# Kernel tuning notes

Hardware: AMD Instinct MI355X
Metric: run time of the kernel (lower is better)

## Reference

```python
import jax, jax.numpy as jnp
import numpy as np

N = 210          # sequence length (== module max_length cap)
DM = 2048        # input feature dim (major and minor)
DK = 1024        # key/query dim
DV = 1024        # value dim
K_CLIP = 32      # relative-position clipping distance


def _make_table(n, k):
    # table[i, j] = clip(j - i, -k, k) + k  (Shaw-style relative position index)
    rel = np.arange(n)[None, :] - np.arange(n)[:, None]
    return jnp.asarray(np.clip(rel, -k, k) + k, dtype=jnp.int32)


def setup_inputs() -> dict:
    key = jax.random.key(0)
    ks = jax.random.split(key, 7)
    X_major = jax.random.normal(ks[0], (N, DM), dtype=jnp.float32)
    X_minor = jax.random.normal(ks[1], (N, DM), dtype=jnp.float32)
    # Linear weights stored as [in, out] for x @ W
    s = 0.02
    Wq = jax.random.normal(ks[2], (DM, DK), dtype=jnp.float32) * s
    Wk = jax.random.normal(ks[3], (DM, DK), dtype=jnp.float32) * s
    Wv = jax.random.normal(ks[4], (DM, DV), dtype=jnp.float32) * s
    Wo = jax.random.normal(ks[5], (DV, DV), dtype=jnp.float32) * s
    wk = jax.random.normal(ks[6], (2 * K_CLIP + 1, DK), dtype=jnp.float32) * s
    table = _make_table(N, K_CLIP)
    return {"X_major": X_major, "X_minor": X_minor, "Wq": Wq, "Wk": Wk,
            "Wv": Wv, "Wo": Wo, "wk": wk, "table": table}


def reference(X_major, X_minor, Wq, Wk, Wv, Wo, wk, table):
    n = X_major.shape[0]
    scale = 1.0 / jnp.sqrt(jnp.asarray(Wq.shape[1], X_major.dtype))
    Q = X_major @ Wq                     # [n, dk]
    K = X_minor @ Wk                     # [n, dk]
    V = X_minor @ Wv                     # [n, dv]
    Qs = Q * scale
    S = Qs @ K.T                         # [n, n] content scores
    Rk = wk[table[:n, :n]]               # [n, n, dk] gathered rel-pos reps
    Sr = jnp.einsum('id,ijd->ij', Qs, Rk)  # [n, n] relative scores
    A = jax.nn.softmax(S + Sr, axis=-1)  # [n, n]
    Y = (A @ V) @ Wo                     # [n, dv]
    return (Y, A)
```

## Files before the change

### kernel.cpp

```cpp
#include <hip/hip_runtime.h>

typedef short bf16x8 __attribute__((ext_vector_type(8)));
typedef float f32x4 __attribute__((ext_vector_type(4)));

#define MFMA16(a, b, c) __builtin_amdgcn_mfma_f32_16x16x32_bf16(a, b, c, 0, 0, 0)

__device__ inline short f2bf(float f) {
  unsigned u = __builtin_bit_cast(unsigned, f);
  u += 0x7FFFu + ((u >> 16) & 1u);
  return (short)(u >> 16);
}
__device__ inline unsigned pack2(float lo, float hi) {
  unsigned a = __builtin_bit_cast(unsigned, lo) + 0x8000u;
  unsigned b = __builtin_bit_cast(unsigned, hi) + 0x8000u;
  return __builtin_amdgcn_perm(b, a, 0x07060302u);
}

__device__ inline void async_cp16(const void* g, void* l) {
  __builtin_amdgcn_global_load_lds(
      (const __attribute__((address_space(1))) unsigned int*)g,
      (__attribute__((address_space(3))) unsigned int*)l, 16, 0, 0);
}

#define SWZ(r, c) ((((r) << 4) + ((c) ^ ((r) & 7))) << 3)


__global__ __launch_bounds__(256) void k_prep(const float* __restrict__ xmaj,
                                              const float* __restrict__ xmin,
                                              const float* __restrict__ wkin,
                                              const float* __restrict__ Wq,
                                              const float* __restrict__ Wk,
                                              const float* __restrict__ Wv,
                                              const float* __restrict__ Wo,
                                              short* __restrict__ xmaj_bf,
                                              short* __restrict__ xmin_bf,
                                              short* __restrict__ kwb,
                                              short* __restrict__ wqt,
                                              short* __restrict__ wkt,
                                              short* __restrict__ wvt,
                                              short* __restrict__ wot) {
  __shared__ short tile[64][72];
  int b = blockIdx.x, t = threadIdx.x;
  if (b < 512) {
    int idx = b * 256 + t;
    if (idx < 107520) {
      float4 v = ((const float4*)xmaj)[idx];
      ((uint2*)xmaj_bf)[idx] = make_uint2(pack2(v.x, v.y), pack2(v.z, v.w));
      float4 u = ((const float4*)xmin)[idx];
      ((uint2*)xmin_bf)[idx] = make_uint2(pack2(u.x, u.y), pack2(u.z, u.w));
    }
    if (idx < 16640) {
      float4 v = ((const float4*)wkin)[idx];
      ((uint2*)(kwb + 210 * 1024))[idx] = make_uint2(pack2(v.x, v.y), pack2(v.z, v.w));
    }
    if (idx < 1664) ((uint4*)(kwb + 275 * 1024))[idx] = make_uint4(0, 0, 0, 0);
    return;
  }
  const float* W;
  short* Wt;
  int kt, nt, dstK;
  if (b < 2048) {
    int wi = (b - 512) >> 9, tl = (b - 512) & 511;
    W = wi == 0 ? Wq : (wi == 1 ? Wk : Wv);
    Wt = wi == 0 ? wqt : (wi == 1 ? wkt : wvt);
    kt = tl >> 4; nt = tl & 15; dstK = 2048;
  } else {
    int tl = b - 2048;
    W = Wo; Wt = wot; kt = tl >> 4; nt = tl & 15; dstK = 1024;
  }
  int k0 = kt * 64, n0 = nt * 64;
  int kp = t >> 4, nl4 = (t & 15) * 4;
  for (int h = 0; h < 2; ++h) {
    int kpp = kp + h * 16;
    const float* g = W + (size_t)(k0 + 2 * kpp) * 1024 + n0 + nl4;
    float4 u = *(const float4*)g;
    float4 v = *(const float4*)(g + 1024);
    *(unsigned*)&tile[nl4 + 0][2 * kpp] = pack2(u.x, v.x);
    *(unsigned*)&tile[nl4 + 1][2 * kpp] = pack2(u.y, v.y);
    *(unsigned*)&tile[nl4 + 2][2 * kpp] = pack2(u.z, v.z);
    *(unsigned*)&tile[nl4 + 3][2 * kpp] = pack2(u.w, v.w);
  }
  __syncthreads();
  int nl = t >> 2, cq = t & 3;
  for (int h = 0; h < 2; ++h) {
    int c = cq + h * 4;
    *(uint4*)(Wt + (size_t)(n0 + nl) * dstK + k0 + c * 8) = *(const uint4*)&tile[nl][c * 8];
  }
}

__global__ __launch_bounds__(256, 1) void k_qkv(const short* __restrict__ xmaj,
                                                const short* __restrict__ xmin,
                                                const short* __restrict__ wqt,
                                                const short* __restrict__ wkt,
                                                const short* __restrict__ wvt,
                                                short* __restrict__ qs,
                                                short* __restrict__ kwb,
                                                short* __restrict__ vt) {
  __shared__ short As[64 * 128];
  __shared__ short Bs[64 * 128];
  int b = blockIdx.x, t = threadIdx.x;
  int x = b & 7, s = b >> 3;
  int ntile = x * 6 + (s >> 2), mtile = s & 3;
  int nn0 = ntile * 64;
  int mat = nn0 >> 10, ncol0 = nn0 & 1023, m0 = mtile * 64;
  const short* A = (mat == 0) ? xmaj : xmin;
  const short* Bt = (mat == 0) ? wqt : (mat == 1 ? wkt : wvt);
  int lane = t & 63, w = t >> 6;
  int wm = w >> 1, wn = w & 1;
  int l15 = lane & 15, l4 = lane >> 4;
  f32x4 acc[2][2] = {};

  for (int k0 = 0; k0 < 2048; k0 += 128) {
    __syncthreads();
#pragma unroll
    for (int j = 0; j < 4; ++j) {
      int sj = t + j * 256;
      int r = sj >> 4, cg = (sj & 15) ^ (r & 7);
      async_cp16(A + (size_t)(m0 + r) * 2048 + k0 + cg * 8, &As[(w * 64 + j * 256) * 8]);
    }
#pragma unroll
    for (int j = 0; j < 4; ++j) {
      int sj = t + j * 256;
      int r = sj >> 4, cg = (sj & 15) ^ (r & 7);
      async_cp16(Bt + (size_t)(ncol0 + r) * 2048 + k0 + cg * 8, &Bs[(w * 64 + j * 256) * 8]);
    }
    __syncthreads();
#pragma unroll
    for (int kk = 0; kk < 4; ++kk) {
      int c = kk * 4 + l4;
      int ra0 = wm * 32 + l15, ra1 = ra0 + 16;
      int rb0 = wn * 32 + l15, rb1 = rb0 + 16;
      bf16x8 a0 = *(const bf16x8*)&As[SWZ(ra0, c)];
      bf16x8 a1 = *(const bf16x8*)&As[SWZ(ra1, c)];
      bf16x8 b0 = *(const bf16x8*)&Bs[SWZ(rb0, c)];
      bf16x8 b1 = *(const bf16x8*)&Bs[SWZ(rb1, c)];
      acc[0][0] = MFMA16(a0, b0, acc[0][0]);
      acc[0][1] = MFMA16(a0, b1, acc[0][1]);
      acc[1][0] = MFMA16(a1, b0, acc[1][0]);
      acc[1][1] = MFMA16(a1, b1, acc[1][1]);
    }
  }

  if (mat < 2) {
    float scale = (mat == 0) ? 0.03125f : 1.0f;
    short* dst = (mat == 0) ? qs : kwb;
#pragma unroll
    for (int mi = 0; mi < 2; ++mi)
#pragma unroll
      for (int ni = 0; ni < 2; ++ni) {
        int r0 = m0 + wm * 32 + mi * 16 + l4 * 4;
        int c = ncol0 + wn * 32 + ni * 16 + l15;
        for (int j = 0; j < 4; ++j) {
          int r = r0 + j;
          if (r < 210) dst[r * 1024 + c] = f2bf(acc[mi][ni][j] * scale);
        }
      }
  } else {
    __syncthreads();
#pragma unroll
    for (int mi = 0; mi < 2; ++mi)
#pragma unroll
      for (int ni = 0; ni < 2; ++ni) {
        int nl = wn * 32 + ni * 16 + l15;
        int ml0 = wm * 32 + mi * 16 + l4 * 4;
        for (int j = 0; j < 4; ++j) As[nl * 72 + ml0 + j] = f2bf(acc[mi][ni][j]);
      }
    __syncthreads();
    for (int h = 0; h < 2; ++h) {
      int idx = t + h * 256;
      int nl = idx >> 3, c8 = idx & 7;
      int mg0 = m0 + c8 * 8;
      short* dstp = vt + (ncol0 + nl) * 256 + mg0;
      if (mg0 + 8 <= 210) {
        *(uint4*)dstp = *(const uint4*)&As[nl * 72 + c8 * 8];
      } else {
        for (int e = 0; e < 8; ++e)
          if (mg0 + e < 210) dstp[e] = As[nl * 72 + c8 * 8 + e];
      }
    }
  }
}

__global__ __launch_bounds__(256, 1) void k_sprime(const short* __restrict__ qs,
                                                   const short* __restrict__ kwb,
                                                   float* __restrict__ Sp) {
  __shared__ short As[32 * 128];
  __shared__ short Bs[64 * 128];
  int n0 = blockIdx.x * 64, m0 = blockIdx.y * 32;
  int t = threadIdx.x, lane = t & 63, w = t >> 6;
  int l15 = lane & 15, l4 = lane >> 4;
  f32x4 acc[2] = {};

  for (int k0 = 0; k0 < 1024; k0 += 128) {
    __syncthreads();
#pragma unroll
    for (int j = 0; j < 2; ++j) {
      int sj = t + j * 256;
      int r = sj >> 4, cg = (sj & 15) ^ (r & 7);
      async_cp16(qs + (size_t)(m0 + r) * 1024 + k0 + cg * 8, &As[(w * 64 + j * 256) * 8]);
    }
#pragma unroll
    for (int j = 0; j < 4; ++j) {
      int sj = t + j * 256;
      int r = sj >> 4, cg = (sj & 15) ^ (r & 7);
      async_cp16(kwb + (size_t)(n0 + r) * 1024 + k0 + cg * 8, &Bs[(w * 64 + j * 256) * 8]);
    }
    __syncthreads();
#pragma unroll
    for (int kk = 0; kk < 4; ++kk) {
      int c = kk * 4 + l4;
      int rb = w * 16 + l15;
      bf16x8 a0 = *(const bf16x8*)&As[SWZ(l15, c)];
      bf16x8 a1 = *(const bf16x8*)&As[SWZ(16 + l15, c)];
      bf16x8 bb = *(const bf16x8*)&Bs[SWZ(rb, c)];
      acc[0] = MFMA16(a0, bb, acc[0]);
      acc[1] = MFMA16(a1, bb, acc[1]);
    }
  }
#pragma unroll
  for (int mi = 0; mi < 2; ++mi) {
    int r0 = m0 + mi * 16 + l4 * 4;
    int col = n0 + w * 16 + l15;
    for (int j = 0; j < 4; ++j) Sp[(r0 + j) * 320 + col] = acc[mi][j];
  }
}

__global__ __launch_bounds__(256) void k_softmax(const float* __restrict__ Sp,
                                                 const int* __restrict__ table,
                                                 short* __restrict__ Abf,
                                                 float* __restrict__ outA) {
  int i = blockIdx.x, t = threadIdx.x;
  if (i >= 210) {
    Abf[i * 256 + t] = 0;
    return;
  }
  __shared__ float srow[288];
  __shared__ float red[4];
  for (int j = t; j < 288; j += 256) srow[j] = Sp[i * 320 + j];
  __syncthreads();
  float logit = -1e30f;
  if (t < 210) {
    int tb = table[i * 210 + t];
    logit = srow[t] + srow[210 + tb];
  }
  float m = logit;
  for (int o = 32; o; o >>= 1) m = fmaxf(m, __shfl_xor(m, o));
  if ((t & 63) == 0) red[t >> 6] = m;
  __syncthreads();
  m = fmaxf(fmaxf(red[0], red[1]), fmaxf(red[2], red[3]));
  float e = (t < 210) ? __expf(logit - m) : 0.0f;
  float s = e;
  for (int o = 32; o; o >>= 1) s += __shfl_xor(s, o);
  __syncthreads();
  if ((t & 63) == 0) red[t >> 6] = s;
  __syncthreads();
  s = red[0] + red[1] + red[2] + red[3];
  float a = e / s;
  Abf[i * 256 + t] = (t < 210) ? f2bf(a) : (short)0;
  if (t < 210) outA[i * 210 + t] = a;
}

__global__ __launch_bounds__(256, 1) void k_av(const short* __restrict__ Abf,
                                               const short* __restrict__ vt,
                                               short* __restrict__ av) {
  __shared__ short As[64 * 128];
  __shared__ short Bs[64 * 128];
  int n0 = blockIdx.x * 64, m0 = blockIdx.y * 64;
  int t = threadIdx.x, lane = t & 63, w = t >> 6;
  int wm = w >> 1, wn = w & 1;
  int l15 = lane & 15, l4 = lane >> 4;
  f32x4 acc[2][2] = {};

  for (int k0 = 0; k0 < 256; k0 += 128) {
    __syncthreads();
#pragma unroll
    for (int j = 0; j < 4; ++j) {
      int sj = t + j * 256;
      int r = sj >> 4, cg = (sj & 15) ^ (r & 7);
      async_cp16(Abf + (size_t)(m0 + r) * 256 + k0 + cg * 8, &As[(w * 64 + j * 256) * 8]);
      async_cp16(vt + (size_t)(n0 + r) * 256 + k0 + cg * 8, &Bs[(w * 64 + j * 256) * 8]);
    }
    __syncthreads();
#pragma unroll
    for (int kk = 0; kk < 4; ++kk) {
      int c = kk * 4 + l4;
      int ra0 = wm * 32 + l15, ra1 = ra0 + 16;
      int rb0 = wn * 32 + l15, rb1 = rb0 + 16;
      bf16x8 a0 = *(const bf16x8*)&As[SWZ(ra0, c)];
      bf16x8 a1 = *(const bf16x8*)&As[SWZ(ra1, c)];
      bf16x8 b0 = *(const bf16x8*)&Bs[SWZ(rb0, c)];
      bf16x8 b1 = *(const bf16x8*)&Bs[SWZ(rb1, c)];
      acc[0][0] = MFMA16(a0, b0, acc[0][0]);
      acc[0][1] = MFMA16(a0, b1, acc[0][1]);
      acc[1][0] = MFMA16(a1, b0, acc[1][0]);
      acc[1][1] = MFMA16(a1, b1, acc[1][1]);
    }
  }
#pragma unroll
  for (int mi = 0; mi < 2; ++mi)
#pragma unroll
    for (int ni = 0; ni < 2; ++ni) {
      int r0 = m0 + wm * 32 + mi * 16 + l4 * 4;
      int c = n0 + wn * 32 + ni * 16 + l15;
      for (int j = 0; j < 4; ++j) {
        int r = r0 + j;
        if (r < 210) av[r * 1024 + c] = f2bf(acc[mi][ni][j]);
      }
    }
}

__global__ __launch_bounds__(256, 1) void k_y(const short* __restrict__ av,
                                              const short* __restrict__ wot,
                                              float* __restrict__ outY) {
  __shared__ short As[64 * 128];
  __shared__ short Bs[64 * 128];
  int n0 = blockIdx.x * 64, m0 = blockIdx.y * 64;
  int t = threadIdx.x, lane = t & 63, w = t >> 6;
  int wm = w >> 1, wn = w & 1;
  int l15 = lane & 15, l4 = lane >> 4;
  f32x4 acc[2][2] = {};

  for (int k0 = 0; k0 < 1024; k0 += 128) {
    __syncthreads();
#pragma unroll
    for (int j = 0; j < 4; ++j) {
      int sj = t + j * 256;
      int r = sj >> 4, cg = (sj & 15) ^ (r & 7);
      async_cp16(av + (size_t)(m0 + r) * 1024 + k0 + cg * 8, &As[(w * 64 + j * 256) * 8]);
      async_cp16(wot + (size_t)(n0 + r) * 1024 + k0 + cg * 8, &Bs[(w * 64 + j * 256) * 8]);
    }
    __syncthreads();
#pragma unroll
    for (int kk = 0; kk < 4; ++kk) {
      int c = kk * 4 + l4;
      int ra0 = wm * 32 + l15, ra1 = ra0 + 16;
      int rb0 = wn * 32 + l15, rb1 = rb0 + 16;
      bf16x8 a0 = *(const bf16x8*)&As[SWZ(ra0, c)];
      bf16x8 a1 = *(const bf16x8*)&As[SWZ(ra1, c)];
      bf16x8 b0 = *(const bf16x8*)&Bs[SWZ(rb0, c)];
      bf16x8 b1 = *(const bf16x8*)&Bs[SWZ(rb1, c)];
      acc[0][0] = MFMA16(a0, b0, acc[0][0]);
      acc[0][1] = MFMA16(a0, b1, acc[0][1]);
      acc[1][0] = MFMA16(a1, b0, acc[1][0]);
      acc[1][1] = MFMA16(a1, b1, acc[1][1]);
    }
  }
#pragma unroll
  for (int mi = 0; mi < 2; ++mi)
#pragma unroll
    for (int ni = 0; ni < 2; ++ni) {
      int r0 = m0 + wm * 32 + mi * 16 + l4 * 4;
      int c = n0 + wn * 32 + ni * 16 + l15;
      for (int j = 0; j < 4; ++j) {
        int r = r0 + j;
        if (r < 210) outY[r * 1024 + c] = acc[mi][ni][j];
      }
    }
}

extern "C" void kernel_launch(void* const* d_in, const int* in_sizes, int n_in,
                              void* d_out, int out_size, void* d_ws, size_t ws_size,
                              hipStream_t stream) {
  const float* Xmaj = (const float*)d_in[0];
  const float* Xmin = (const float*)d_in[1];
  const float* Wq = (const float*)d_in[2];
  const float* Wk = (const float*)d_in[3];
  const float* Wv = (const float*)d_in[4];
  const float* Wo = (const float*)d_in[5];
  const float* wk = (const float*)d_in[6];
  const int* table = (const int*)d_in[7];

  char* ws = (char*)d_ws;
  short* xmaj_bf = (short*)(ws + 0);
  short* xmin_bf = (short*)(ws + 1048576);
  short* qs = (short*)(ws + 2097152);
  short* kwb = (short*)(ws + 2621440);
  short* vt = (short*)(ws + 3276800);
  short* Abf = (short*)(ws + 3801088);
  short* av = (short*)(ws + 3932160);
  float* Sp = (float*)(ws + 4456448);
  short* wqt = (short*)(ws + 4743168);
  short* wkt = (short*)(ws + 8937472);
  short* wvt = (short*)(ws + 13131776);
  short* wot = (short*)(ws + 17326080);

  float* outY = (float*)d_out;
  float* outA = (float*)d_out + 215040;

  k_prep<<<2304, 256, 0, stream>>>(Xmaj, Xmin, wk, Wq, Wk, Wv, Wo,
                                   xmaj_bf, xmin_bf, kwb, wqt, wkt, wvt, wot);
  k_qkv<<<192, 256, 0, stream>>>(xmaj_bf, xmin_bf, wqt, wkt, wvt, qs, kwb, vt);
  k_sprime<<<dim3(5, 7), 256, 0, stream>>>(qs, kwb, Sp);
  k_softmax<<<256, 256, 0, stream>>>(Sp, table, Abf, outA);
  k_av<<<dim3(16, 4), 256, 0, stream>>>(Abf, vt, av);
  k_y<<<dim3(16, 4), 256, 0, stream>>>(av, wot, outY);
}
```

Baseline: 127.0 us.

## Fuse softmax into AV GEMM and double K-tile depth to 256

Removes the separate softmax kernel. Each AV block now computes the softmax rows for its 64-row tile directly from Sp and the table, writes them into LDS as bf16, and writes the fp32 A output only from the blocks with n0==0. All GEMM kernels (qkv, sprime, y) also move from 128-wide to 256-wide K tiles, using a new 32-chunk swizzle, which halves the number of loop iterations and barriers. In exchange, each of the 16 column blocks recomputes softmax for its rows, and LDS use per block grows considerably (about 118KB in the fused kernel).

```diff
diff --git a/kernel.cpp b/kernel.cpp
--- a/kernel.cpp
+++ b/kernel.cpp
@@ -15,14 +15,14 @@
   unsigned b = __builtin_bit_cast(unsigned, hi) + 0x8000u;
   return __builtin_amdgcn_perm(b, a, 0x07060302u);
 }
-
 __device__ inline void async_cp16(const void* g, void* l) {
   __builtin_amdgcn_global_load_lds(
       (const __attribute__((address_space(1))) unsigned int*)g,
       (__attribute__((address_space(3))) unsigned int*)l, 16, 0, 0);
 }
-
-#define SWZ(r, c) ((((r) << 4) + ((c) ^ ((r) & 7))) << 3)
+__device__ inline int swz5(int r, int c) {
+  return ((r << 5) + ((c & ~7) | ((c ^ r) & 7))) << 3;
+}
 
 
 __global__ __launch_bounds__(256) void k_prep(const float* __restrict__ xmaj,
@@ -96,8 +96,8 @@
                                                 short* __restrict__ qs,
                                                 short* __restrict__ kwb,
                                                 short* __restrict__ vt) {
-  __shared__ short As[64 * 128];
-  __shared__ short Bs[64 * 128];
+  __shared__ short As[64 * 256];
+  __shared__ short Bs[64 * 256];
   int b = blockIdx.x, t = threadIdx.x;
   int x = b & 7, s = b >> 3;
   int ntile = x * 6 + (s >> 2), mtile = s & 3;
@@ -110,30 +110,32 @@
   int l15 = lane & 15, l4 = lane >> 4;
   f32x4 acc[2][2] = {};
 
-  for (int k0 = 0; k0 < 2048; k0 += 128) {
-    __syncthreads();
-#pragma unroll
-    for (int j = 0; j < 4; ++j) {
+  for (int k0 = 0; k0 < 2048; k0 += 256) {
+    __syncthreads();
+#pragma unroll
+    for (int j = 0; j < 8; ++j) {
       int sj = t + j * 256;
-      int r = sj >> 4, cg = (sj & 15) ^ (r & 7);
-      async_cp16(A + (size_t)(m0 + r) * 2048 + k0 + cg * 8, &As[(w * 64 + j * 256) * 8]);
-    }
-#pragma unroll
-    for (int j = 0; j < 4; ++j) {
+      int r = sj >> 5, c = sj & 31;
+      int cg = (c & ~7) | ((c ^ r) & 7);
+      async_cp16(A + (size_t)(m0 + r) * 2048 + k0 + cg * 8, &As[(j * 256 + w * 64) * 8]);
+    }
+#pragma unroll
+    for (int j = 0; j < 8; ++j) {
       int sj = t + j * 256;
-      int r = sj >> 4, cg = (sj & 15) ^ (r & 7);
-      async_cp16(Bt + (size_t)(ncol0 + r) * 2048 + k0 + cg * 8, &Bs[(w * 64 + j * 256) * 8]);
-    }
-    __syncthreads();
-#pragma unroll
-    for (int kk = 0; kk < 4; ++kk) {
+      int r = sj >> 5, c = sj & 31;
+      int cg = (c & ~7) | ((c ^ r) & 7);
+      async_cp16(Bt + (size_t)(ncol0 + r) * 2048 + k0 + cg * 8, &Bs[(j * 256 + w * 64) * 8]);
+    }
+    __syncthreads();
+#pragma unroll
+    for (int kk = 0; kk < 8; ++kk) {
       int c = kk * 4 + l4;
       int ra0 = wm * 32 + l15, ra1 = ra0 + 16;
       int rb0 = wn * 32 + l15, rb1 = rb0 + 16;
-      bf16x8 a0 = *(const bf16x8*)&As[SWZ(ra0, c)];
-      bf16x8 a1 = *(const bf16x8*)&As[SWZ(ra1, c)];
-      bf16x8 b0 = *(const bf16x8*)&Bs[SWZ(rb0, c)];
-      bf16x8 b1 = *(const bf16x8*)&Bs[SWZ(rb1, c)];
+      bf16x8 a0 = *(const bf16x8*)&As[swz5(ra0, c)];
+      bf16x8 a1 = *(const bf16x8*)&As[swz5(ra1, c)];
+      bf16x8 b0 = *(const bf16x8*)&Bs[swz5(rb0, c)];
+      bf16x8 b1 = *(const bf16x8*)&Bs[swz5(rb1, c)];
       acc[0][0] = MFMA16(a0, b0, acc[0][0]);
       acc[0][1] = MFMA16(a0, b1, acc[0][1]);
       acc[1][0] = MFMA16(a1, b0, acc[1][0]);
@@ -184,35 +186,36 @@
 __global__ __launch_bounds__(256, 1) void k_sprime(const short* __restrict__ qs,
                                                    const short* __restrict__ kwb,
                                                    float* __restrict__ Sp) {
-  __shared__ short As[32 * 128];
-  __shared__ short Bs[64 * 128];
+  __shared__ short As2[32 * 256];
+  __shared__ short Bs2[64 * 256];
   int n0 = blockIdx.x * 64, m0 = blockIdx.y * 32;
   int t = threadIdx.x, lane = t & 63, w = t >> 6;
   int l15 = lane & 15, l4 = lane >> 4;
   f32x4 acc[2] = {};
 
-  for (int k0 = 0; k0 < 1024; k0 += 128) {
-    __syncthreads();
-#pragma unroll
-    for (int j = 0; j < 2; ++j) {
-      int sj = t + j * 256;
-      int r = sj >> 4, cg = (sj & 15) ^ (r & 7);
-      async_cp16(qs + (size_t)(m0 + r) * 1024 + k0 + cg * 8, &As[(w * 64 + j * 256) * 8]);
-    }
+  for (int k0 = 0; k0 < 1024; k0 += 256) {
+    __syncthreads();
 #pragma unroll
     for (int j = 0; j < 4; ++j) {
       int sj = t + j * 256;
-      int r = sj >> 4, cg = (sj & 15) ^ (r & 7);
-      async_cp16(kwb + (size_t)(n0 + r) * 1024 + k0 + cg * 8, &Bs[(w * 64 + j * 256) * 8]);
-    }
-    __syncthreads();
-#pragma unroll
-    for (int kk = 0; kk < 4; ++kk) {
+      int r = sj >> 5, c = sj & 31;
+      int cg = (c & ~7) | ((c ^ r) & 7);
+      async_cp16(qs + (size_t)(m0 + r) * 1024 + k0 + cg * 8, &As2[(j * 256 + w * 64) * 8]);
+    }
+#pragma unroll
+    for (int j = 0; j < 8; ++j) {
+      int sj = t + j * 256;
+      int r = sj >> 5, c = sj & 31;
+      int cg = (c & ~7) | ((c ^ r) & 7);
+      async_cp16(kwb + (size_t)(n0 + r) * 1024 + k0 + cg * 8, &Bs2[(j * 256 + w * 64) * 8]);
+    }
+    __syncthreads();
+#pragma unroll
+    for (int kk = 0; kk < 8; ++kk) {
       int c = kk * 4 + l4;
-      int rb = w * 16 + l15;
-      bf16x8 a0 = *(const bf16x8*)&As[SWZ(l15, c)];
-      bf16x8 a1 = *(const bf16x8*)&As[SWZ(16 + l15, c)];
-      bf16x8 bb = *(const bf16x8*)&Bs[SWZ(rb, c)];
+      bf16x8 a0 = *(const bf16x8*)&As2[swz5(l15, c)];
+      bf16x8 a1 = *(const bf16x8*)&As2[swz5(16 + l15, c)];
+      bf16x8 bb = *(const bf16x8*)&Bs2[swz5(w * 16 + l15, c)];
       acc[0] = MFMA16(a0, bb, acc[0]);
       acc[1] = MFMA16(a1, bb, acc[1]);
     }
@@ -225,120 +228,123 @@
   }
 }
 
-__global__ __launch_bounds__(256) void k_softmax(const float* __restrict__ Sp,
-                                                 const int* __restrict__ table,
-                                                 short* __restrict__ Abf,
-                                                 float* __restrict__ outA) {
-  int i = blockIdx.x, t = threadIdx.x;
-  if (i >= 210) {
-    Abf[i * 256 + t] = 0;
-    return;
-  }
-  __shared__ float srow[288];
-  __shared__ float red[4];
-  for (int j = t; j < 288; j += 256) srow[j] = Sp[i * 320 + j];
+__global__ __launch_bounds__(256, 1) void k_av_smax(const float* __restrict__ Sp,
+                                                    const int* __restrict__ table,
+                                                    const short* __restrict__ vt,
+                                                    short* __restrict__ av,
+                                                    float* __restrict__ outA) {
+  __shared__ short As[64 * 256];
+  __shared__ short Bs[64 * 256];
+  __shared__ float Ls[64 * 212];
+  int n0 = blockIdx.x * 64, m0 = blockIdx.y * 64;
+  int t = threadIdx.x, lane = t & 63, w = t >> 6;
+  int wm = w >> 1, wn = w & 1;
+  int l15 = lane & 15, l4 = lane >> 4;
+
+#pragma unroll
+  for (int j = 0; j < 8; ++j) {
+    int sj = t + j * 256;
+    int r = sj >> 5, c = sj & 31;
+    int cg = (c & ~7) | ((c ^ r) & 7);
+    async_cp16(vt + (size_t)(n0 + r) * 256 + cg * 8, &Bs[(j * 256 + w * 64) * 8]);
+  }
+
+  int r = t >> 2, q = t & 3;
+  int row = m0 + r;
+  float* Lr = Ls + r * 212;
+  if (row < 210) {
+    const float* sp = Sp + (size_t)row * 320;
+    const int* tr = table + (size_t)row * 210;
+    float mx = -1e30f;
+    for (int j = q; j < 210; j += 4) {
+      int tb = tr[j];
+      float lg = sp[j] + sp[210 + tb];
+      Lr[j] = lg;
+      mx = fmaxf(mx, lg);
+    }
+    for (int o = 2; o; o >>= 1) mx = fmaxf(mx, __shfl_xor(mx, o, 4));
+    float sum = 0.0f;
+    for (int j = q; j < 210; j += 4) {
+      float e = __expf(Lr[j] - mx);
+      Lr[j] = e;
+      sum += e;
+    }
+    for (int o = 2; o; o >>= 1) sum += __shfl_xor(sum, o, 4);
+    float inv = 1.0f / sum;
+    bool wA = (n0 == 0);
+    for (int j = q; j < 256; j += 4) {
+      if (j < 210) {
+        float a = Lr[j] * inv;
+        As[swz5(r, j >> 3) + (j & 7)] = f2bf(a);
+        if (wA) outA[(size_t)row * 210 + j] = a;
+      } else {
+        As[swz5(r, j >> 3) + (j & 7)] = 0;
+      }
+    }
+  } else {
+    for (int j = q; j < 256; j += 4) As[swz5(r, j >> 3) + (j & 7)] = 0;
+  }
   __syncthreads();
-  float logit = -1e30f;
-  if (t < 210) {
-    int tb = table[i * 210 + t];
-    logit = srow[t] + srow[210 + tb];
-  }
-  float m = logit;
-  for (int o = 32; o; o >>= 1) m = fmaxf(m, __shfl_xor(m, o));
-  if ((t & 63) == 0) red[t >> 6] = m;
-  __syncthreads();
-  m = fmaxf(fmaxf(red[0], red[1]), fmaxf(red[2], red[3]));
-  float e = (t < 210) ? __expf(logit - m) : 0.0f;
-  float s = e;
-  for (int o = 32; o; o >>= 1) s += __shfl_xor(s, o);
-  __syncthreads();
-  if ((t & 63) == 0) red[t >> 6] = s;
-  __syncthreads();
-  s = red[0] + red[1] + red[2] + red[3];
-  float a = e / s;
-  Abf[i * 256 + t] = (t < 210) ? f2bf(a) : (short)0;
-  if (t < 210) outA[i * 210 + t] = a;
-}
-
-__global__ __launch_bounds__(256, 1) void k_av(const short* __restrict__ Abf,
-                                               const short* __restrict__ vt,
-                                               short* __restrict__ av) {
-  __shared__ short As[64 * 128];
-  __shared__ short Bs[64 * 128];
+
+  f32x4 acc[2][2] = {};
+#pragma unroll
+  for (int kk = 0; kk < 8; ++kk) {
+    int c = kk * 4 + l4;
+    int ra0 = wm * 32 + l15, ra1 = ra0 + 16;
+    int rb0 = wn * 32 + l15, rb1 = rb0 + 16;
+    bf16x8 a0 = *(const bf16x8*)&As[swz5(ra0, c)];
+    bf16x8 a1 = *(const bf16x8*)&As[swz5(ra1, c)];
+    bf16x8 b0 = *(const bf16x8*)&Bs[swz5(rb0, c)];
+    bf16x8 b1 = *(const bf16x8*)&Bs[swz5(rb1, c)];
+    acc[0][0] = MFMA16(a0, b0, acc[0][0]);
+    acc[0][1] = MFMA16(a0, b1, acc[0][1]);
+    acc[1][0] = MFMA16(a1, b0, acc[1][0]);
+    acc[1][1] = MFMA16(a1, b1, acc[1][1]);
+  }
+#pragma unroll
+  for (int mi = 0; mi < 2; ++mi)
+#pragma unroll
+    for (int ni = 0; ni < 2; ++ni) {
+      int r0 = m0 + wm * 32 + mi * 16 + l4 * 4;
+      int c = n0 + wn * 32 + ni * 16 + l15;
+      for (int j = 0; j < 4; ++j) {
+        int rr = r0 + j;
+        if (rr < 210) av[rr * 1024 + c] = f2bf(acc[mi][ni][j]);
+      }
+    }
+}
+
+__global__ __launch_bounds__(256, 1) void k_y(const short* __restrict__ av,
+                                              const short* __restrict__ wot,
+                                              float* __restrict__ outY) {
+  __shared__ short As[64 * 256];
+  __shared__ short Bs[64 * 256];
   int n0 = blockIdx.x * 64, m0 = blockIdx.y * 64;
   int t = threadIdx.x, lane = t & 63, w = t >> 6;
   int wm = w >> 1, wn = w & 1;
   int l15 = lane & 15, l4 = lane >> 4;
   f32x4 acc[2][2] = {};
 
-  for (int k0 = 0; k0 < 256; k0 += 128) {
-    __syncthreads();
-#pragma unroll
-    for (int j = 0; j < 4; ++j) {
+  for (int k0 = 0; k0 < 1024; k0 += 256) {
+    __syncthreads();
+#pragma unroll
+    for (int j = 0; j < 8; ++j) {
       int sj = t + j * 256;
-      int r = sj >> 4, cg = (sj & 15) ^ (r & 7);
-      async_cp16(Abf + (size_t)(m0 + r) * 256 + k0 + cg * 8, &As[(w * 64 + j * 256) * 8]);
-      async_cp16(vt + (size_t)(n0 + r) * 256 + k0 + cg * 8, &Bs[(w * 64 + j * 256) * 8]);
-    }
-    __syncthreads();
-#pragma unroll
-    for (int kk = 0; kk < 4; ++kk) {
+      int r = sj >> 5, c = sj & 31;
+      int cg = (c & ~7) | ((c ^ r) & 7);
+      async_cp16(av + (size_t)(m0 + r) * 1024 + k0 + cg * 8, &As[(j * 256 + w * 64) * 8]);
+      async_cp16(wot + (size_t)(n0 + r) * 1024 + k0 + cg * 8, &Bs[(j * 256 + w * 64) * 8]);
+    }
+    __syncthreads();
+#pragma unroll
+    for (int kk = 0; kk < 8; ++kk) {
       int c = kk * 4 + l4;
       int ra0 = wm * 32 + l15, ra1 = ra0 + 16;
       int rb0 = wn * 32 + l15, rb1 = rb0 + 16;
-      bf16x8 a0 = *(const bf16x8*)&As[SWZ(ra0, c)];
-      bf16x8 a1 = *(const bf16x8*)&As[SWZ(ra1, c)];
-      bf16x8 b0 = *(const bf16x8*)&Bs[SWZ(rb0, c)];
-      bf16x8 b1 = *(const bf16x8*)&Bs[SWZ(rb1, c)];
-      acc[0][0] = MFMA16(a0, b0, acc[0][0]);
-      acc[0][1] = MFMA16(a0, b1, acc[0][1]);
-      acc[1][0] = MFMA16(a1, b0, acc[1][0]);
-      acc[1][1] = MFMA16(a1, b1, acc[1][1]);
-    }
-  }
-#pragma unroll
-  for (int mi = 0; mi < 2; ++mi)
-#pragma unroll
-    for (int ni = 0; ni < 2; ++ni) {
-      int r0 = m0 + wm * 32 + mi * 16 + l4 * 4;
-      int c = n0 + wn * 32 + ni * 16 + l15;
-      for (int j = 0; j < 4; ++j) {
-        int r = r0 + j;
-        if (r < 210) av[r * 1024 + c] = f2bf(acc[mi][ni][j]);
-      }
-    }
-}
-
-__global__ __launch_bounds__(256, 1) void k_y(const short* __restrict__ av,
-                                              const short* __restrict__ wot,
-                                              float* __restrict__ outY) {
-  __shared__ short As[64 * 128];
-  __shared__ short Bs[64 * 128];
-  int n0 = blockIdx.x * 64, m0 = blockIdx.y * 64;
-  int t = threadIdx.x, lane = t & 63, w = t >> 6;
-  int wm = w >> 1, wn = w & 1;
-  int l15 = lane & 15, l4 = lane >> 4;
-  f32x4 acc[2][2] = {};
-
-  for (int k0 = 0; k0 < 1024; k0 += 128) {
-    __syncthreads();
-#pragma unroll
-    for (int j = 0; j < 4; ++j) {
-      int sj = t + j * 256;
-      int r = sj >> 4, cg = (sj & 15) ^ (r & 7);
-      async_cp16(av + (size_t)(m0 + r) * 1024 + k0 + cg * 8, &As[(w * 64 + j * 256) * 8]);
-      async_cp16(wot + (size_t)(n0 + r) * 1024 + k0 + cg * 8, &Bs[(w * 64 + j * 256) * 8]);
-    }
-    __syncthreads();
-#pragma unroll
-    for (int kk = 0; kk < 4; ++kk) {
-      int c = kk * 4 + l4;
-      int ra0 = wm * 32 + l15, ra1 = ra0 + 16;
-      int rb0 = wn * 32 + l15, rb1 = rb0 + 16;
-      bf16x8 a0 = *(const bf16x8*)&As[SWZ(ra0, c)];
-      bf16x8 a1 = *(const bf16x8*)&As[SWZ(ra1, c)];
-      bf16x8 b0 = *(const bf16x8*)&Bs[SWZ(rb0, c)];
-      bf16x8 b1 = *(const bf16x8*)&Bs[SWZ(rb1, c)];
+      bf16x8 a0 = *(const bf16x8*)&As[swz5(ra0, c)];
+      bf16x8 a1 = *(const bf16x8*)&As[swz5(ra1, c)];
+      bf16x8 b0 = *(const bf16x8*)&Bs[swz5(rb0, c)];
+      bf16x8 b1 = *(const bf16x8*)&Bs[swz5(rb1, c)];
       acc[0][0] = MFMA16(a0, b0, acc[0][0]);
       acc[0][1] = MFMA16(a0, b1, acc[0][1]);
       acc[1][0] = MFMA16(a1, b0, acc[1][0]);
@@ -376,7 +382,6 @@
   short* qs = (short*)(ws + 2097152);
   short* kwb = (short*)(ws + 2621440);
   short* vt = (short*)(ws + 3276800);
-  short* Abf = (short*)(ws + 3801088);
   short* av = (short*)(ws + 3932160);
   float* Sp = (float*)(ws + 4456448);
   short* wqt = (short*)(ws + 4743168);
@@ -391,7 +396,6 @@
                                    xmaj_bf, xmin_bf, kwb, wqt, wkt, wvt, wot);
   k_qkv<<<192, 256, 0, stream>>>(xmaj_bf, xmin_bf, wqt, wkt, wvt, qs, kwb, vt);
   k_sprime<<<dim3(5, 7), 256, 0, stream>>>(qs, kwb, Sp);
-  k_softmax<<<256, 256, 0, stream>>>(Sp, table, Abf, outA);
-  k_av<<<dim3(16, 4), 256, 0, stream>>>(Abf, vt, av);
+  k_av_smax<<<dim3(16, 4), 256, 0, stream>>>(Sp, table, vt, av, outA);
   k_y<<<dim3(16, 4), 256, 0, stream>>>(av, wot, outY);
 }
```

Result: slower. 150.9 us (+18.8%).

## Fuse fp32-to-bf16 conversion into QKV GEMM and double-buffer GEMM loads

Applied to the files above, without the earlier changes.

Removes the separate prep kernel. The QKV GEMM now loads fp32 X and W tiles straight into LDS with async copies, converts them to bf16 in-kernel, and transposes W through LDS. Extra blocks of the same launch handle the wk conversion and the Wo transpose. The sprime and y kernels gain double-buffered LDS prefetch, and k_av loads its whole K=256 extent in one shot. This avoids a full fp32-to-bf16 round trip through global memory for the large weights, at the cost of more LDS use and conversion work repeated inside each GEMM block.

```diff
diff --git a/kernel.cpp b/kernel.cpp
--- a/kernel.cpp
+++ b/kernel.cpp
@@ -15,129 +15,146 @@
   unsigned b = __builtin_bit_cast(unsigned, hi) + 0x8000u;
   return __builtin_amdgcn_perm(b, a, 0x07060302u);
 }
-
 __device__ inline void async_cp16(const void* g, void* l) {
   __builtin_amdgcn_global_load_lds(
       (const __attribute__((address_space(1))) unsigned int*)g,
       (__attribute__((address_space(3))) unsigned int*)l, 16, 0, 0);
 }
-
 #define SWZ(r, c) ((((r) << 4) + ((c) ^ ((r) & 7))) << 3)
-
-
-__global__ __launch_bounds__(256) void k_prep(const float* __restrict__ xmaj,
-                                              const float* __restrict__ xmin,
-                                              const float* __restrict__ wkin,
-                                              const float* __restrict__ Wq,
-                                              const float* __restrict__ Wk,
-                                              const float* __restrict__ Wv,
-                                              const float* __restrict__ Wo,
-                                              short* __restrict__ xmaj_bf,
-                                              short* __restrict__ xmin_bf,
-                                              short* __restrict__ kwb,
-                                              short* __restrict__ wqt,
-                                              short* __restrict__ wkt,
-                                              short* __restrict__ wvt,
-                                              short* __restrict__ wot) {
-  __shared__ short tile[64][72];
-  int b = blockIdx.x, t = threadIdx.x;
-  if (b < 512) {
-    int idx = b * 256 + t;
-    if (idx < 107520) {
-      float4 v = ((const float4*)xmaj)[idx];
-      ((uint2*)xmaj_bf)[idx] = make_uint2(pack2(v.x, v.y), pack2(v.z, v.w));
-      float4 u = ((const float4*)xmin)[idx];
-      ((uint2*)xmin_bf)[idx] = make_uint2(pack2(u.x, u.y), pack2(u.z, u.w));
-    }
-    if (idx < 16640) {
-      float4 v = ((const float4*)wkin)[idx];
-      ((uint2*)(kwb + 210 * 1024))[idx] = make_uint2(pack2(v.x, v.y), pack2(v.z, v.w));
-    }
-    if (idx < 1664) ((uint4*)(kwb + 275 * 1024))[idx] = make_uint4(0, 0, 0, 0);
-    return;
-  }
-  const float* W;
-  short* Wt;
-  int kt, nt, dstK;
-  if (b < 2048) {
-    int wi = (b - 512) >> 9, tl = (b - 512) & 511;
-    W = wi == 0 ? Wq : (wi == 1 ? Wk : Wv);
-    Wt = wi == 0 ? wqt : (wi == 1 ? wkt : wvt);
-    kt = tl >> 4; nt = tl & 15; dstK = 2048;
-  } else {
-    int tl = b - 2048;
-    W = Wo; Wt = wot; kt = tl >> 4; nt = tl & 15; dstK = 1024;
-  }
-  int k0 = kt * 64, n0 = nt * 64;
-  int kp = t >> 4, nl4 = (t & 15) * 4;
-  for (int h = 0; h < 2; ++h) {
-    int kpp = kp + h * 16;
-    const float* g = W + (size_t)(k0 + 2 * kpp) * 1024 + n0 + nl4;
-    float4 u = *(const float4*)g;
-    float4 v = *(const float4*)(g + 1024);
-    *(unsigned*)&tile[nl4 + 0][2 * kpp] = pack2(u.x, v.x);
-    *(unsigned*)&tile[nl4 + 1][2 * kpp] = pack2(u.y, v.y);
-    *(unsigned*)&tile[nl4 + 2][2 * kpp] = pack2(u.z, v.z);
-    *(unsigned*)&tile[nl4 + 3][2 * kpp] = pack2(u.w, v.w);
-  }
-  __syncthreads();
-  int nl = t >> 2, cq = t & 3;
-  for (int h = 0; h < 2; ++h) {
-    int c = cq + h * 4;
-    *(uint4*)(Wt + (size_t)(n0 + nl) * dstK + k0 + c * 8) = *(const uint4*)&tile[nl][c * 8];
-  }
-}
-
-__global__ __launch_bounds__(256, 1) void k_qkv(const short* __restrict__ xmaj,
-                                                const short* __restrict__ xmin,
-                                                const short* __restrict__ wqt,
-                                                const short* __restrict__ wkt,
-                                                const short* __restrict__ wvt,
+__device__ inline int swz5(int r, int c) {
+  return ((r << 5) + ((c & ~7) | ((c ^ r) & 7))) << 3;
+}
+__device__ inline int xsw(int r, int c) { return (c & ~7) | ((c ^ r) & 7); }
+
+
+__global__ __launch_bounds__(256, 1) void k_qkv(const float* __restrict__ xmaj,
+                                                const float* __restrict__ xmin,
+                                                const float* __restrict__ Wq,
+                                                const float* __restrict__ Wk,
+                                                const float* __restrict__ Wv,
+                                                const float* __restrict__ Wo,
+                                                const float* __restrict__ wkin,
                                                 short* __restrict__ qs,
                                                 short* __restrict__ kwb,
-                                                short* __restrict__ vt) {
-  __shared__ short As[64 * 128];
+                                                short* __restrict__ vt,
+                                                short* __restrict__ wot) {
+  __shared__ float Xs[2][64 * 128];
+  __shared__ float Ws[2][128 * 64];
   __shared__ short Bs[64 * 128];
   int b = blockIdx.x, t = threadIdx.x;
+
+  if (b >= 192) {
+    if (b < 194) {
+      int idx = (b - 192) * 256 + t;
+      const float4* src = (const float4*)wkin;
+      uint2* dst = (uint2*)(kwb + 210 * 1024);
+      for (int i = idx; i < 16640; i += 512) {
+        float4 v = src[i];
+        dst[i] = make_uint2(pack2(v.x, v.y), pack2(v.z, v.w));
+      }
+      for (int i = idx; i < 1664; i += 512)
+        ((uint4*)(kwb + 275 * 1024))[i] = make_uint4(0, 0, 0, 0);
+    } else {
+      short(*tile)[72] = (short(*)[72])Bs;
+      int tl = b - 194;
+      int k0 = (tl >> 4) * 64, n0 = (tl & 15) * 64;
+      int kp = t >> 4, nl4 = (t & 15) * 4;
+#pragma unroll
+      for (int h = 0; h < 2; ++h) {
+        int kpp = kp + h * 16;
+        const float* g = Wo + (size_t)(k0 + 2 * kpp) * 1024 + n0 + nl4;
+        float4 u = *(const float4*)g;
+        float4 v = *(const float4*)(g + 1024);
+        *(unsigned*)&tile[nl4 + 0][2 * kpp] = pack2(u.x, v.x);
+        *(unsigned*)&tile[nl4 + 1][2 * kpp] = pack2(u.y, v.y);
+        *(unsigned*)&tile[nl4 + 2][2 * kpp] = pack2(u.z, v.z);
+        *(unsigned*)&tile[nl4 + 3][2 * kpp] = pack2(u.w, v.w);
+      }
+      __syncthreads();
+      int nl = t >> 2, cq = t & 3;
+#pragma unroll
+      for (int h = 0; h < 2; ++h) {
+        int c = cq + h * 4;
+        *(uint4*)(wot + (size_t)(n0 + nl) * 1024 + k0 + c * 8) = *(const uint4*)&tile[nl][c * 8];
+      }
+    }
+    return;
+  }
+
   int x = b & 7, s = b >> 3;
   int ntile = x * 6 + (s >> 2), mtile = s & 3;
   int nn0 = ntile * 64;
   int mat = nn0 >> 10, ncol0 = nn0 & 1023, m0 = mtile * 64;
-  const short* A = (mat == 0) ? xmaj : xmin;
-  const short* Bt = (mat == 0) ? wqt : (mat == 1 ? wkt : wvt);
+  const float* Xa = (mat == 0) ? xmaj : xmin;
+  const float* Wp = (mat == 0) ? Wq : (mat == 1 ? Wk : Wv);
   int lane = t & 63, w = t >> 6;
   int wm = w >> 1, wn = w & 1;
   int l15 = lane & 15, l4 = lane >> 4;
   f32x4 acc[2][2] = {};
 
-  for (int k0 = 0; k0 < 2048; k0 += 128) {
+  auto issue = [&](int p) {
+    int k0 = p * 128;
+    float* X = &Xs[p & 1][0];
+    float* W2 = &Ws[p & 1][0];
+#pragma unroll
+    for (int j = 0; j < 8; ++j) {
+      int sj = t + j * 256;
+      int r = sj >> 5, c = sj & 31;
+      int row = m0 + r;
+      row = row > 209 ? 209 : row;
+      async_cp16(Xa + (size_t)row * 2048 + k0 + xsw(r, c) * 4, &X[(j * 256 + w * 64) * 4]);
+    }
+#pragma unroll
+    for (int j = 0; j < 8; ++j) {
+      int sj = t + j * 256;
+      int r = sj >> 4, c = sj & 15;
+      async_cp16(Wp + (size_t)(k0 + r) * 1024 + ncol0 + xsw(r, c) * 4, &W2[(j * 256 + w * 64) * 4]);
+    }
+  };
+
+  issue(0);
+#pragma unroll 1
+  for (int p = 0; p < 16; ++p) {
     __syncthreads();
-#pragma unroll
-    for (int j = 0; j < 4; ++j) {
-      int sj = t + j * 256;
-      int r = sj >> 4, cg = (sj & 15) ^ (r & 7);
-      async_cp16(A + (size_t)(m0 + r) * 2048 + k0 + cg * 8, &As[(w * 64 + j * 256) * 8]);
-    }
-#pragma unroll
-    for (int j = 0; j < 4; ++j) {
-      int sj = t + j * 256;
-      int r = sj >> 4, cg = (sj & 15) ^ (r & 7);
-      async_cp16(Bt + (size_t)(ncol0 + r) * 2048 + k0 + cg * 8, &Bs[(w * 64 + j * 256) * 8]);
-    }
-    __syncthreads();
-#pragma unroll
-    for (int kk = 0; kk < 4; ++kk) {
-      int c = kk * 4 + l4;
-      int ra0 = wm * 32 + l15, ra1 = ra0 + 16;
-      int rb0 = wn * 32 + l15, rb1 = rb0 + 16;
-      bf16x8 a0 = *(const bf16x8*)&As[SWZ(ra0, c)];
-      bf16x8 a1 = *(const bf16x8*)&As[SWZ(ra1, c)];
-      bf16x8 b0 = *(const bf16x8*)&Bs[SWZ(rb0, c)];
-      bf16x8 b1 = *(const bf16x8*)&Bs[SWZ(rb1, c)];
-      acc[0][0] = MFMA16(a0, b0, acc[0][0]);
-      acc[0][1] = MFMA16(a0, b1, acc[0][1]);
-      acc[1][0] = MFMA16(a1, b0, acc[1][0]);
-      acc[1][1] = MFMA16(a1, b1, acc[1][1]);
+    if (p < 15) issue(p + 1);
+    {
+      const float* W2 = &Ws[p & 1][0];
+#pragma unroll
+      for (int h = 0; h < 4; ++h) {
+        int kp = (t >> 4) + 16 * h, nq = t & 15;
+        int r0 = 2 * kp, r1 = r0 + 1;
+        float4 u = *(const float4*)&W2[r0 * 64 + xsw(r0, nq) * 4];
+        float4 v = *(const float4*)&W2[r1 * 64 + xsw(r1, nq) * 4];
+        int kc = kp >> 2, e = r0 & 7;
+        *(unsigned*)&Bs[SWZ(nq * 4 + 0, kc) + e] = pack2(u.x, v.x);
+        *(unsigned*)&Bs[SWZ(nq * 4 + 1, kc) + e] = pack2(u.y, v.y);
+        *(unsigned*)&Bs[SWZ(nq * 4 + 2, kc) + e] = pack2(u.z, v.z);
+        *(unsigned*)&Bs[SWZ(nq * 4 + 3, kc) + e] = pack2(u.w, v.w);
+      }
+    }
+    asm volatile("s_waitcnt lgkmcnt(0)\ns_barrier" ::: "memory");
+    {
+      const float* X = &Xs[p & 1][0];
+#pragma unroll
+      for (int kk = 0; kk < 4; ++kk) {
+        int c = kk * 4 + l4;
+        int ra0 = wm * 32 + l15, ra1 = ra0 + 16;
+        int rb0 = wn * 32 + l15, rb1 = rb0 + 16;
+        float4 u0 = *(const float4*)&X[ra0 * 128 + xsw(ra0, 2 * c) * 4];
+        float4 v0 = *(const float4*)&X[ra0 * 128 + xsw(ra0, 2 * c + 1) * 4];
+        float4 u1 = *(const float4*)&X[ra1 * 128 + xsw(ra1, 2 * c) * 4];
+        float4 v1 = *(const float4*)&X[ra1 * 128 + xsw(ra1, 2 * c + 1) * 4];
+        uint4 pa0 = make_uint4(pack2(u0.x, u0.y), pack2(u0.z, u0.w), pack2(v0.x, v0.y), pack2(v0.z, v0.w));
+        uint4 pa1 = make_uint4(pack2(u1.x, u1.y), pack2(u1.z, u1.w), pack2(v1.x, v1.y), pack2(v1.z, v1.w));
+        bf16x8 a0 = __builtin_bit_cast(bf16x8, pa0);
+        bf16x8 a1 = __builtin_bit_cast(bf16x8, pa1);
+        bf16x8 b0 = *(const bf16x8*)&Bs[SWZ(rb0, c)];
+        bf16x8 b1 = *(const bf16x8*)&Bs[SWZ(rb1, c)];
+        acc[0][0] = MFMA16(a0, b0, acc[0][0]);
+        acc[0][1] = MFMA16(a0, b1, acc[0][1]);
+        acc[1][0] = MFMA16(a1, b0, acc[1][0]);
+        acc[1][1] = MFMA16(a1, b1, acc[1][1]);
+      }
     }
   }
 
@@ -157,13 +174,14 @@
       }
   } else {
     __syncthreads();
+    short* scr = Bs;
 #pragma unroll
     for (int mi = 0; mi < 2; ++mi)
 #pragma unroll
       for (int ni = 0; ni < 2; ++ni) {
         int nl = wn * 32 + ni * 16 + l15;
         int ml0 = wm * 32 + mi * 16 + l4 * 4;
-        for (int j = 0; j < 4; ++j) As[nl * 72 + ml0 + j] = f2bf(acc[mi][ni][j]);
+        for (int j = 0; j < 4; ++j) scr[nl * 72 + ml0 + j] = f2bf(acc[mi][ni][j]);
       }
     __syncthreads();
     for (int h = 0; h < 2; ++h) {
@@ -172,10 +190,10 @@
       int mg0 = m0 + c8 * 8;
       short* dstp = vt + (ncol0 + nl) * 256 + mg0;
       if (mg0 + 8 <= 210) {
-        *(uint4*)dstp = *(const uint4*)&As[nl * 72 + c8 * 8];
+        *(uint4*)dstp = *(const uint4*)&scr[nl * 72 + c8 * 8];
       } else {
         for (int e = 0; e < 8; ++e)
-          if (mg0 + e < 210) dstp[e] = As[nl * 72 + c8 * 8 + e];
+          if (mg0 + e < 210) dstp[e] = scr[nl * 72 + c8 * 8 + e];
       }
     }
   }
@@ -184,35 +202,41 @@
 __global__ __launch_bounds__(256, 1) void k_sprime(const short* __restrict__ qs,
                                                    const short* __restrict__ kwb,
                                                    float* __restrict__ Sp) {
-  __shared__ short As[32 * 128];
-  __shared__ short Bs[64 * 128];
+  __shared__ short As[2][32 * 128];
+  __shared__ short Bs[2][64 * 128];
   int n0 = blockIdx.x * 64, m0 = blockIdx.y * 32;
   int t = threadIdx.x, lane = t & 63, w = t >> 6;
   int l15 = lane & 15, l4 = lane >> 4;
   f32x4 acc[2] = {};
 
-  for (int k0 = 0; k0 < 1024; k0 += 128) {
-    __syncthreads();
+  auto issue = [&](int p) {
+    int k0 = p * 128, d = p & 1;
 #pragma unroll
     for (int j = 0; j < 2; ++j) {
       int sj = t + j * 256;
       int r = sj >> 4, cg = (sj & 15) ^ (r & 7);
-      async_cp16(qs + (size_t)(m0 + r) * 1024 + k0 + cg * 8, &As[(w * 64 + j * 256) * 8]);
+      async_cp16(qs + (size_t)(m0 + r) * 1024 + k0 + cg * 8, &As[d][(j * 256 + w * 64) * 8]);
     }
 #pragma unroll
     for (int j = 0; j < 4; ++j) {
       int sj = t + j * 256;
       int r = sj >> 4, cg = (sj & 15) ^ (r & 7);
-      async_cp16(kwb + (size_t)(n0 + r) * 1024 + k0 + cg * 8, &Bs[(w * 64 + j * 256) * 8]);
-    }
+      async_cp16(kwb + (size_t)(n0 + r) * 1024 + k0 + cg * 8, &Bs[d][(j * 256 + w * 64) * 8]);
+    }
+  };
+
+  issue(0);
+#pragma unroll 1
+  for (int p = 0; p < 8; ++p) {
     __syncthreads();
+    if (p < 7) issue(p + 1);
+    int d = p & 1;
 #pragma unroll
     for (int kk = 0; kk < 4; ++kk) {
       int c = kk * 4 + l4;
-      int rb = w * 16 + l15;
-      bf16x8 a0 = *(const bf16x8*)&As[SWZ(l15, c)];
-      bf16x8 a1 = *(const bf16x8*)&As[SWZ(16 + l15, c)];
-      bf16x8 bb = *(const bf16x8*)&Bs[SWZ(rb, c)];
+      bf16x8 a0 = *(const bf16x8*)&As[d][SWZ(l15, c)];
+      bf16x8 a1 = *(const bf16x8*)&As[d][SWZ(16 + l15, c)];
+      bf16x8 bb = *(const bf16x8*)&Bs[d][SWZ(w * 16 + l15, c)];
       acc[0] = MFMA16(a0, bb, acc[0]);
       acc[1] = MFMA16(a1, bb, acc[1]);
     }
@@ -263,38 +287,37 @@
 __global__ __launch_bounds__(256, 1) void k_av(const short* __restrict__ Abf,
                                                const short* __restrict__ vt,
                                                short* __restrict__ av) {
-  __shared__ short As[64 * 128];
-  __shared__ short Bs[64 * 128];
+  __shared__ short As[64 * 256];
+  __shared__ short Bs[64 * 256];
   int n0 = blockIdx.x * 64, m0 = blockIdx.y * 64;
   int t = threadIdx.x, lane = t & 63, w = t >> 6;
   int wm = w >> 1, wn = w & 1;
   int l15 = lane & 15, l4 = lane >> 4;
+
+#pragma unroll
+  for (int j = 0; j < 8; ++j) {
+    int sj = t + j * 256;
+    int r = sj >> 5, c = sj & 31;
+    int cg = (c & ~7) | ((c ^ r) & 7);
+    async_cp16(Abf + (size_t)(m0 + r) * 256 + cg * 8, &As[(j * 256 + w * 64) * 8]);
+    async_cp16(vt + (size_t)(n0 + r) * 256 + cg * 8, &Bs[(j * 256 + w * 64) * 8]);
+  }
+  __syncthreads();
+
   f32x4 acc[2][2] = {};
-
-  for (int k0 = 0; k0 < 256; k0 += 128) {
-    __syncthreads();
-#pragma unroll
-    for (int j = 0; j < 4; ++j) {
-      int sj = t + j * 256;
-      int r = sj >> 4, cg = (sj & 15) ^ (r & 7);
-      async_cp16(Abf + (size_t)(m0 + r) * 256 + k0 + cg * 8, &As[(w * 64 + j * 256) * 8]);
-      async_cp16(vt + (size_t)(n0 + r) * 256 + k0 + cg * 8, &Bs[(w * 64 + j * 256) * 8]);
-    }
-    __syncthreads();
-#pragma unroll
-    for (int kk = 0; kk < 4; ++kk) {
-      int c = kk * 4 + l4;
-      int ra0 = wm * 32 + l15, ra1 = ra0 + 16;
-      int rb0 = wn * 32 + l15, rb1 = rb0 + 16;
-      bf16x8 a0 = *(const bf16x8*)&As[SWZ(ra0, c)];
-      bf16x8 a1 = *(const bf16x8*)&As[SWZ(ra1, c)];
-      bf16x8 b0 = *(const bf16x8*)&Bs[SWZ(rb0, c)];
-      bf16x8 b1 = *(const bf16x8*)&Bs[SWZ(rb1, c)];
-      acc[0][0] = MFMA16(a0, b0, acc[0][0]);
-      acc[0][1] = MFMA16(a0, b1, acc[0][1]);
-      acc[1][0] = MFMA16(a1, b0, acc[1][0]);
-      acc[1][1] = MFMA16(a1, b1, acc[1][1]);
-    }
+#pragma unroll
+  for (int kk = 0; kk < 8; ++kk) {
+    int c = kk * 4 + l4;
+    int ra0 = wm * 32 + l15, ra1 = ra0 + 16;
+    int rb0 = wn * 32 + l15, rb1 = rb0 + 16;
+    bf16x8 a0 = *(const bf16x8*)&As[swz5(ra0, c)];
+    bf16x8 a1 = *(const bf16x8*)&As[swz5(ra1, c)];
+    bf16x8 b0 = *(const bf16x8*)&Bs[swz5(rb0, c)];
+    bf16x8 b1 = *(const bf16x8*)&Bs[swz5(rb1, c)];
+    acc[0][0] = MFMA16(a0, b0, acc[0][0]);
+    acc[0][1] = MFMA16(a0, b1, acc[0][1]);
+    acc[1][0] = MFMA16(a1, b0, acc[1][0]);
+    acc[1][1] = MFMA16(a1, b1, acc[1][1]);
   }
 #pragma unroll
   for (int mi = 0; mi < 2; ++mi)
@@ -312,33 +335,40 @@
 __global__ __launch_bounds__(256, 1) void k_y(const short* __restrict__ av,
                                               const short* __restrict__ wot,
                                               float* __restrict__ outY) {
-  __shared__ short As[64 * 128];
-  __shared__ short Bs[64 * 128];
+  __shared__ short As[2][64 * 128];
+  __shared__ short Bs[2][64 * 128];
   int n0 = blockIdx.x * 64, m0 = blockIdx.y * 64;
   int t = threadIdx.x, lane = t & 63, w = t >> 6;
   int wm = w >> 1, wn = w & 1;
   int l15 = lane & 15, l4 = lane >> 4;
   f32x4 acc[2][2] = {};
 
-  for (int k0 = 0; k0 < 1024; k0 += 128) {
-    __syncthreads();
+  auto issue = [&](int p) {
+    int k0 = p * 128, d = p & 1;
 #pragma unroll
     for (int j = 0; j < 4; ++j) {
       int sj = t + j * 256;
       int r = sj >> 4, cg = (sj & 15) ^ (r & 7);
-      async_cp16(av + (size_t)(m0 + r) * 1024 + k0 + cg * 8, &As[(w * 64 + j * 256) * 8]);
-      async_cp16(wot + (size_t)(n0 + r) * 1024 + k0 + cg * 8, &Bs[(w * 64 + j * 256) * 8]);
-    }
+      async_cp16(av + (size_t)(m0 + r) * 1024 + k0 + cg * 8, &As[d][(j * 256 + w * 64) * 8]);
+      async_cp16(wot + (size_t)(n0 + r) * 1024 + k0 + cg * 8, &Bs[d][(j * 256 + w * 64) * 8]);
+    }
+  };
+
+  issue(0);
+#pragma unroll 1
+  for (int p = 0; p < 8; ++p) {
     __syncthreads();
+    if (p < 7) issue(p + 1);
+    int d = p & 1;
 #pragma unroll
     for (int kk = 0; kk < 4; ++kk) {
       int c = kk * 4 + l4;
       int ra0 = wm * 32 + l15, ra1 = ra0 + 16;
       int rb0 = wn * 32 + l15, rb1 = rb0 + 16;
-      bf16x8 a0 = *(const bf16x8*)&As[SWZ(ra0, c)];
-      bf16x8 a1 = *(const bf16x8*)&As[SWZ(ra1, c)];
-      bf16x8 b0 = *(const bf16x8*)&Bs[SWZ(rb0, c)];
-      bf16x8 b1 = *(const bf16x8*)&Bs[SWZ(rb1, c)];
+      bf16x8 a0 = *(const bf16x8*)&As[d][SWZ(ra0, c)];
+      bf16x8 a1 = *(const bf16x8*)&As[d][SWZ(ra1, c)];
+      bf16x8 b0 = *(const bf16x8*)&Bs[d][SWZ(rb0, c)];
+      bf16x8 b1 = *(const bf16x8*)&Bs[d][SWZ(rb1, c)];
       acc[0][0] = MFMA16(a0, b0, acc[0][0]);
       acc[0][1] = MFMA16(a0, b1, acc[0][1]);
       acc[1][0] = MFMA16(a1, b0, acc[1][0]);
@@ -371,25 +401,18 @@
   const int* table = (const int*)d_in[7];
 
   char* ws = (char*)d_ws;
-  short* xmaj_bf = (short*)(ws + 0);
-  short* xmin_bf = (short*)(ws + 1048576);
-  short* qs = (short*)(ws + 2097152);
-  short* kwb = (short*)(ws + 2621440);
-  short* vt = (short*)(ws + 3276800);
-  short* Abf = (short*)(ws + 3801088);
-  short* av = (short*)(ws + 3932160);
-  float* Sp = (float*)(ws + 4456448);
-  short* wqt = (short*)(ws + 4743168);
-  short* wkt = (short*)(ws + 8937472);
-  short* wvt = (short*)(ws + 13131776);
-  short* wot = (short*)(ws + 17326080);
+  short* qs = (short*)(ws + 0);
+  short* kwb = (short*)(ws + 524288);
+  short* vt = (short*)(ws + 1179648);
+  short* Abf = (short*)(ws + 1703936);
+  short* av = (short*)(ws + 1835008);
+  float* Sp = (float*)(ws + 2359296);
+  short* wot = (short*)(ws + 2646016);
 
   float* outY = (float*)d_out;
   float* outA = (float*)d_out + 215040;
 
-  k_prep<<<2304, 256, 0, stream>>>(Xmaj, Xmin, wk, Wq, Wk, Wv, Wo,
-                                   xmaj_bf, xmin_bf, kwb, wqt, wkt, wvt, wot);
-  k_qkv<<<192, 256, 0, stream>>>(xmaj_bf, xmin_bf, wqt, wkt, wvt, qs, kwb, vt);
+  k_qkv<<<450, 256, 0, stream>>>(Xmaj, Xmin, Wq, Wk, Wv, Wo, wk, qs, kwb, vt, wot);
   k_sprime<<<dim3(5, 7), 256, 0, stream>>>(qs, kwb, Sp);
   k_softmax<<<256, 256, 0, stream>>>(Sp, table, Abf, outA);
   k_av<<<dim3(16, 4), 256, 0, stream>>>(Abf, vt, av);
```

After: 136.3 us. +7.3%, slower.
